# Kernel optimization log

Measured on AMD Instinct MI355X. Metric: run time of the kernel, lower is better.

Reference implementation:

```python
import jax, jax.numpy as jnp
import numpy as np

N = 67108864  # 64M elements, ~256 MB fp32


def setup_inputs() -> dict:
    key = jax.random.key(0)
    x = jax.random.normal(key, (N,), dtype=jnp.float32)
    return {"x": x, "bins": 256, "min": -4, "max": 4}


def reference(x, bins, min, max):
    # Faithful jnp translation of torch.histc:
    #   bin width = (max - min) / bins
    #   values in [min, max] are counted; x == max falls in the last bin;
    #   values outside the range are dropped. Output dtype matches input (float).
    lo = jnp.float32(min)
    hi = jnp.float32(max)
    width = (hi - lo) / bins
    idx = jnp.floor((x - lo) / width).astype(jnp.int32)
    # right edge is inclusive -> goes to last bin
    idx = jnp.clip(idx, 0, bins - 1)
    in_range = (x >= lo) & (x <= hi)
    w = jnp.where(in_range, jnp.float32(1.0), jnp.float32(0.0))
    hist = jnp.zeros((bins,), dtype=jnp.float32).at[idx].add(w)
    return hist
```

## Files before the change

### kernel.cpp

```cpp
#include <hip/hip_runtime.h>

#define NBINS 256
#define TPB 256
#define NCOPY 4
#define CSTRIDE 264

typedef float f32x4 __attribute__((ext_vector_type(4)));

__global__ void zero_out_kernel(float* __restrict__ out) {
    out[threadIdx.x] = 0.0f;
}

__global__ __launch_bounds__(TPB) void hist_kernel(const float* __restrict__ x,
                                                   float* __restrict__ out,
                                                   int n) {
    __shared__ int lh[NCOPY * CSTRIDE];
    const int tid = threadIdx.x;
    int* __restrict__ myh = &lh[(tid >> 6) * CSTRIDE];

    for (int i = tid; i < NCOPY * CSTRIDE; i += TPB)
        lh[i] = 0;
    __syncthreads();

    const int gid    = blockIdx.x * TPB + tid;
    const int stride = gridDim.x * TPB;
    const int n4     = n >> 2;
    const f32x4* __restrict__ x4 = (const f32x4*)x;

#define PROC(f) {                                        \
        float _t = ((f) + 4.0f) * 32.0f;                 \
        unsigned _u = (unsigned)_t;                      \
        _u = _u > 255u ? 255u : _u;                      \
        bool _ok = __builtin_fabsf(f) <= 4.0f;           \
        int _b = _ok ? (int)_u : 256;                    \
        atomicAdd(&myh[_b], 1);                          \
    }
#define PROC16(a, b, c, d) {                             \
        PROC(a.x) PROC(a.y) PROC(a.z) PROC(a.w)          \
        PROC(b.x) PROC(b.y) PROC(b.z) PROC(b.w)          \
        PROC(c.x) PROC(c.y) PROC(c.z) PROC(c.w)          \
        PROC(d.x) PROC(d.y) PROC(d.z) PROC(d.w)          \
    }

    const int iters = n4 / (4 * stride);

    if (iters > 0) {
        const int wave_gid = (blockIdx.x << 2) | (tid >> 6);
        const int p = wave_gid % iters;

        int t = p;
        int i = gid + t * 4 * stride;
        f32x4 a = __builtin_nontemporal_load(&x4[i]);
        f32x4 b = __builtin_nontemporal_load(&x4[i + stride]);
        f32x4 c = __builtin_nontemporal_load(&x4[i + 2 * stride]);
        f32x4 d = __builtin_nontemporal_load(&x4[i + 3 * stride]);
        for (int k = 1; k < iters; ++k) {
            int tn = t + 1;
            tn = (tn == iters) ? 0 : tn;
            const int ni = gid + tn * 4 * stride;
            f32x4 na = __builtin_nontemporal_load(&x4[ni]);
            f32x4 nb = __builtin_nontemporal_load(&x4[ni + stride]);
            f32x4 nc = __builtin_nontemporal_load(&x4[ni + 2 * stride]);
            f32x4 nd = __builtin_nontemporal_load(&x4[ni + 3 * stride]);
            PROC16(a, b, c, d)
            a = na; b = nb; c = nc; d = nd;
            t = tn;
        }
        PROC16(a, b, c, d)
    }

    for (int i = iters * 4 * stride + gid; i < n4; i += stride) {
        f32x4 a = __builtin_nontemporal_load(&x4[i]);
        PROC(a.x) PROC(a.y) PROC(a.z) PROC(a.w)
    }
    for (int j = (n4 << 2) + gid; j < n; j += stride) {
        float f = x[j];
        PROC(f)
    }
#undef PROC16
#undef PROC

    __syncthreads();

    int s = lh[0 * CSTRIDE + tid] + lh[1 * CSTRIDE + tid] +
            lh[2 * CSTRIDE + tid] + lh[3 * CSTRIDE + tid];
    if (s)
        atomicAdd(&out[tid], (float)s);
}

extern "C" void kernel_launch(void* const* d_in, const int* in_sizes, int n_in,
                              void* d_out, int out_size, void* d_ws, size_t ws_size,
                              hipStream_t stream) {
    const float* x = (const float*)d_in[0];
    float* out = (float*)d_out;
    const int n = in_sizes[0];

    zero_out_kernel<<<1, NBINS, 0, stream>>>(out);

    int n4 = n >> 2;
    long long want = ((long long)n4 + (long long)TPB * 4 - 1) / ((long long)TPB * 4);
    int blocks = (int)(want < 1 ? 1 : (want > 2048 ? 2048 : want));
    hist_kernel<<<blocks, TPB, 0, stream>>>(x, out, n);
}
```

Baseline: 78.08 us.

## Give each wave a contiguous 4KB chunk, drop nontemporal loads, double grid

```diff
diff --git a/kernel.cpp b/kernel.cpp
--- a/kernel.cpp
+++ b/kernel.cpp
@@ -22,9 +22,10 @@
         lh[i] = 0;
     __syncthreads();
 
-    const int gid    = blockIdx.x * TPB + tid;
-    const int stride = gridDim.x * TPB;
-    const int n4     = n >> 2;
+    const int lane = tid & 63;
+    const int w    = (blockIdx.x << 2) | (tid >> 6);
+    const int W    = gridDim.x << 2;
+    const int n4   = n >> 2;
     const f32x4* __restrict__ x4 = (const f32x4*)x;
 
 #define PROC(f) {                                        \
@@ -42,38 +43,35 @@
         PROC(d.x) PROC(d.y) PROC(d.z) PROC(d.w)          \
     }
 
-    const int iters = n4 / (4 * stride);
+    const int iters = n4 / (W << 8);
 
     if (iters > 0) {
-        const int wave_gid = (blockIdx.x << 2) | (tid >> 6);
-        const int p = wave_gid % iters;
-
-        int t = p;
-        int i = gid + t * 4 * stride;
-        f32x4 a = __builtin_nontemporal_load(&x4[i]);
-        f32x4 b = __builtin_nontemporal_load(&x4[i + stride]);
-        f32x4 c = __builtin_nontemporal_load(&x4[i + 2 * stride]);
-        f32x4 d = __builtin_nontemporal_load(&x4[i + 3 * stride]);
-        for (int k = 1; k < iters; ++k) {
-            int tn = t + 1;
-            tn = (tn == iters) ? 0 : tn;
-            const int ni = gid + tn * 4 * stride;
-            f32x4 na = __builtin_nontemporal_load(&x4[ni]);
-            f32x4 nb = __builtin_nontemporal_load(&x4[ni + stride]);
-            f32x4 nc = __builtin_nontemporal_load(&x4[ni + 2 * stride]);
-            f32x4 nd = __builtin_nontemporal_load(&x4[ni + 3 * stride]);
+        int base = w << 8;
+        const int step = W << 8;
+        f32x4 a = x4[base + lane];
+        f32x4 b = x4[base + 64 + lane];
+        f32x4 c = x4[base + 128 + lane];
+        f32x4 d = x4[base + 192 + lane];
+        for (int t = 1; t < iters; ++t) {
+            const int nb = base + step;
+            f32x4 na = x4[nb + lane];
+            f32x4 nb2 = x4[nb + 64 + lane];
+            f32x4 nc = x4[nb + 128 + lane];
+            f32x4 nd = x4[nb + 192 + lane];
             PROC16(a, b, c, d)
-            a = na; b = nb; c = nc; d = nd;
-            t = tn;
+            a = na; b = nb2; c = nc; d = nd;
+            base = nb;
         }
         PROC16(a, b, c, d)
     }
 
-    for (int i = iters * 4 * stride + gid; i < n4; i += stride) {
-        f32x4 a = __builtin_nontemporal_load(&x4[i]);
+    for (int i = iters * (W << 8) + blockIdx.x * TPB + tid; i < n4;
+         i += gridDim.x * TPB) {
+        f32x4 a = x4[i];
         PROC(a.x) PROC(a.y) PROC(a.z) PROC(a.w)
     }
-    for (int j = (n4 << 2) + gid; j < n; j += stride) {
+    for (int j = (n4 << 2) + blockIdx.x * TPB + tid; j < n;
+         j += gridDim.x * TPB) {
         float f = x[j];
         PROC(f)
     }
@@ -98,7 +96,7 @@
     zero_out_kernel<<<1, NBINS, 0, stream>>>(out);
 
     int n4 = n >> 2;
-    long long want = ((long long)n4 + (long long)TPB * 4 - 1) / ((long long)TPB * 4);
-    int blocks = (int)(want < 1 ? 1 : (want > 2048 ? 2048 : want));
+    long long want = ((long long)n4 + 1023) / 1024;
+    int blocks = (int)(want < 1 ? 1 : (want > 4096 ? 4096 : want));
     hist_kernel<<<blocks, TPB, 0, stream>>>(x, out, n);
 }
```

After: 117.5 us (median of 2 runs). 1.51x slower.
